# Kernel tuning notes

Measured on AMD Instinct MI355X. Metric: run time of the kernel, lower is better.

## Reference

```python
import jax, jax.numpy as jnp
import numpy as np
import math

B, N, C = 4, 4096, 1024
H, K_LM = 16, 256
HEAD_DIM = C // H


def setup_inputs() -> dict:
    key = jax.random.key(0)
    k1, k2, k3, k4, k5 = jax.random.split(key, 5)
    x = jax.random.normal(k1, (B, N, C), dtype=jnp.float32)
    Wqkv = jax.random.normal(k2, (3 * C, C), dtype=jnp.float32) * 0.02
    E = jax.random.normal(k3, (H, K_LM, N), dtype=jnp.float32) * 0.02
    Wproj = jax.random.normal(k4, (C, C), dtype=jnp.float32) * 0.02
    bproj = jax.random.normal(k5, (C,), dtype=jnp.float32) * 0.02
    return {"x": x, "Wqkv": Wqkv, "E": E, "Wproj": Wproj, "bproj": bproj}


def reference(x, Wqkv, E, Wproj, bproj):
    Bsz, n, c = x.shape
    h, d = H, c // H
    # qkv projection (no bias): [B,N,3C] -> (3,B,H,N,d)
    qkv = (x @ Wqkv.T).reshape(Bsz, n, 3, h, d).transpose(2, 0, 3, 1, 4)
    q, k, v = qkv[0], qkv[1], qkv[2]
    # Linformer landmark projection: E[h,k,n] @ K/V[b,h,n,d] -> [b,h,k,d]
    k_lm = jnp.einsum('hkn,bhnd->bhkd', E, k)
    v_lm = jnp.einsum('hkn,bhnd->bhkd', E, v)
    # scaled dot + softmax over landmarks: [b,h,n,k]
    dot = jnp.einsum('bhnd,bhkd->bhnk', q, k_lm) / math.sqrt(d)
    attn = jax.nn.softmax(dot, axis=-1)
    # weighted sum; faithful to original: reshape (B,H,N,d) -> (B,N,C) WITHOUT head transpose
    out = jnp.einsum('bhnk,bhkd->bhnd', attn, v_lm).reshape(Bsz, n, c)
    # output projection (dropouts are identity at eval / p=0)
    return out @ Wproj.T + bproj
```

## Files before the change

### kernel.cpp

```cpp
#include <hip/hip_runtime.h>


typedef unsigned short ushort_t;
typedef float f32x4 __attribute__((ext_vector_type(4)));
typedef __bf16 bf16x8 __attribute__((ext_vector_type(8)));
typedef unsigned short ushort8 __attribute__((ext_vector_type(8)));
typedef unsigned short ushort4_t __attribute__((ext_vector_type(4)));

__device__ inline ushort_t f2bf(float f) {
  unsigned int u = __float_as_uint(f);
  u += 0x7fff + ((u >> 16) & 1);
  return (ushort_t)(u >> 16);
}

__device__ inline void gload_lds16(const ushort_t* g, ushort_t* l) {
  __builtin_amdgcn_global_load_lds(
      (const __attribute__((address_space(1))) void*)g,
      (__attribute__((address_space(3))) void*)l, 16, 0, 0);
}

__global__ __launch_bounds__(256) void cvt_all(
    const float* __restrict__ x,  ushort_t* __restrict__ xo,
    const float* __restrict__ w1, ushort_t* __restrict__ w1o,
    const float* __restrict__ e,  ushort_t* __restrict__ eo,
    const float* __restrict__ w2, ushort_t* __restrict__ w2o) {
  int i = blockIdx.x * blockDim.x + threadIdx.x;
  const float* in; ushort_t* out; int idx;
  if (i < 4194304)               { in = x;  out = xo;  idx = i; }
  else if (i < 4980736)          { in = w1; out = w1o; idx = i - 4194304; }
  else if (i < 9175040)          { in = e;  out = eo;  idx = i - 4980736; }
  else                           { in = w2; out = w2o; idx = i - 9175040; }
  float4 v = ((const float4*)in)[idx];
  ushort4_t o;
  o.x = f2bf(v.x); o.y = f2bf(v.y); o.z = f2bf(v.z); o.w = f2bf(v.w);
  ((ushort4_t*)out)[idx] = o;
}


#define BARX __builtin_amdgcn_s_barrier()
#define WVM(n) do { asm volatile("s_waitcnt vmcnt(" #n ")" ::: "memory"); \
                    __builtin_amdgcn_sched_barrier(0); } while (0)
#define WLG  do { asm volatile("s_waitcnt lgkmcnt(0)" ::: "memory"); \
                  __builtin_amdgcn_sched_barrier(0); } while (0)

#define STG_A(h, slot, tt) do { \
    gload_lds16(sA[h][0] + (tt) * 64, (ushort_t*)(smem + (slot) * 32768 + (h) * 16384 + (w * 2 + 0) * 1024)); \
    gload_lds16(sA[h][1] + (tt) * 64, (ushort_t*)(smem + (slot) * 32768 + (h) * 16384 + (w * 2 + 1) * 1024)); \
  } while (0)
#define STG_B(h, slot, tt) do { \
    gload_lds16(sB[h][0] + (tt) * 64, (ushort_t*)(smem + 65536 + (slot) * 32768 + (h) * 16384 + (w * 2 + 0) * 1024)); \
    gload_lds16(sB[h][1] + (tt) * 64, (ushort_t*)(smem + 65536 + (slot) * 32768 + (h) * 16384 + (w * 2 + 1) * 1024)); \
  } while (0)

#define RD_A(mh, AF) do { \
    const char* ba_ = smem + sl * 32768 + ((mh) * 128 + wm * 64 + l15) * 128; \
    _Pragma("unroll") for (int i_ = 0; i_ < 4; i_++) { \
      AF[i_][0] = *(const bf16x8*)(ba_ + i_ * 2048 + cs0); \
      AF[i_][1] = *(const bf16x8*)(ba_ + i_ * 2048 + cs1); } \
  } while (0)
#define RD_B(nh) do { \
    const char* bb_ = smem + 65536 + sl * 32768 + ((nh) * 128 + wn * 32 + l15) * 128; \
    _Pragma("unroll") for (int j_ = 0; j_ < 2; j_++) { \
      bF[j_][0] = *(const bf16x8*)(bb_ + j_ * 2048 + cs0); \
      bF[j_][1] = *(const bf16x8*)(bb_ + j_ * 2048 + cs1); } \
  } while (0)

#define MQ(mh, nh, AF) do { \
    _Pragma("unroll") for (int i_ = 0; i_ < 4; i_++) \
    _Pragma("unroll") for (int j_ = 0; j_ < 2; j_++) { \
      acc[(mh) * 4 + i_][(nh) * 2 + j_] = __builtin_amdgcn_mfma_f32_16x16x32_bf16( \
          AF[i_][0], bF[j_][0], acc[(mh) * 4 + i_][(nh) * 2 + j_], 0, 0, 0); \
      acc[(mh) * 4 + i_][(nh) * 2 + j_] = __builtin_amdgcn_mfma_f32_16x16x32_bf16( \
          AF[i_][1], bF[j_][1], acc[(mh) * 4 + i_][(nh) * 2 + j_], 0, 0, 0); } \
  } while (0)

__device__ __attribute__((always_inline)) inline void pipe256(
    const ushort_t* __restrict__ Ag, const ushort_t* __restrict__ Bg,
    long long m0, long long n0, char* smem, f32x4 acc[8][4]) {
  const int tid = threadIdx.x, lane = tid & 63, w = tid >> 6;
  const int l15 = lane & 15, quad = lane >> 4;
  const int wm = w >> 2, wn = w & 3;
  const int sw = l15 & 7;
  const int K = 1024;
  const int cs0 = ((0 * 4 + quad) ^ sw) << 4;
  const int cs1 = ((1 * 4 + quad) ^ sw) << 4;
  const int lr8 = lane >> 3;
  const int sdat = ((lane & 7) ^ lr8) * 8;
  const ushort_t* sA[2][2];
  const ushort_t* sB[2][2];
#pragma unroll
  for (int h = 0; h < 2; h++)
#pragma unroll
    for (int q = 0; q < 2; q++) {
      sA[h][q] = Ag + (m0 + h * 128 + (w * 2 + q) * 8 + lr8) * K + sdat;
      sB[h][q] = Bg + (n0 + h * 128 + (w * 2 + q) * 8 + lr8) * K + sdat;
    }

  const f32x4 zz = {0.f, 0.f, 0.f, 0.f};
#pragma unroll
  for (int i = 0; i < 8; i++)
#pragma unroll
    for (int j = 0; j < 4; j++) acc[i][j] = zz;

  bf16x8 aF0[4][2];
  bf16x8 aF1[4][2];
  bf16x8 bF[2][2];

  STG_A(0, 0, 0); STG_B(0, 0, 0); STG_A(1, 0, 0); STG_B(1, 0, 0);
  WVM(4);
  BARX;

#pragma unroll 2
  for (int t = 0; t < 16; ++t) {
    const int sl = t & 1, sn = sl ^ 1;
    const bool pf = (t < 15);
    RD_A(0, aF0); RD_B(0);
    if (pf) STG_A(0, sn, t + 1);
    BARX; WLG;
    __builtin_amdgcn_s_setprio(1); MQ(0, 0, aF0); __builtin_amdgcn_s_setprio(0);
    if (pf) { WVM(4); } else { WVM(2); }
    BARX;
    RD_A(1, aF1);
    if (pf) STG_B(0, sn, t + 1);
    BARX; WLG;
    __builtin_amdgcn_s_setprio(1); MQ(1, 0, aF1); __builtin_amdgcn_s_setprio(0);
    if (pf) { WVM(4); } else { WVM(0); }
    BARX;
    RD_B(1);
    if (pf) STG_A(1, sn, t + 1);
    BARX; WLG;
    __builtin_amdgcn_s_setprio(1); MQ(1, 1, aF1); __builtin_amdgcn_s_setprio(0);
    BARX;
    if (pf) STG_B(1, sn, t + 1);
    BARX; WLG;
    __builtin_amdgcn_s_setprio(1); MQ(0, 1, aF0); __builtin_amdgcn_s_setprio(0);
    if (pf) WVM(4);
    BARX;
  }
}

__global__ __launch_bounds__(512) void gemm_qkv(
    const ushort_t* __restrict__ A, const ushort_t* __restrict__ W,
    ushort_t* __restrict__ q, ushort_t* __restrict__ kT, ushort_t* __restrict__ vT) {
  __shared__ __align__(16) char smem[131072];
  const int lin = blockIdx.x;
  const int xcd = lin & 7, rr_ = lin >> 3;
  const int mt = xcd * 8 + (rr_ & 7);
  const int nt = rr_ >> 3;
  const long long m0 = (long long)mt * 256;
  const long long n0 = (long long)nt * 256;

  f32x4 acc[8][4];
  pipe256(A, W, m0, n0, smem, acc);

  const int tid = threadIdx.x, lane = tid & 63, w = tid >> 6;
  const int l15 = lane & 15, quad = lane >> 4;
  const int wm = w >> 2, wn = w & 3;
  const int b     = (int)(m0 >> 12);
  const int nrow0 = (int)(m0 & 4095);
  const int s     = (int)(n0 >> 10);
  const int ncol0 = (int)(n0 & 1023);
  const int h0    = ncol0 >> 6;

  if (s == 0) {
#pragma unroll
    for (int mh = 0; mh < 2; mh++)
#pragma unroll
      for (int i = 0; i < 4; i++)
#pragma unroll
        for (int nh = 0; nh < 2; nh++)
#pragma unroll
          for (int j = 0; j < 2; j++) {
            int cx = ncol0 + nh * 128 + wn * 32 + j * 16;
            int h  = cx >> 6;
            int dd = (cx & 63) + l15;
            long long z = (long long)b * 16 + h;
            int nb = nrow0 + mh * 128 + wm * 64 + i * 16 + quad * 4;
#pragma unroll
            for (int r = 0; r < 4; r++)
              q[z * 262144 + (long long)(nb + r) * 64 + dd] = f2bf(acc[mh * 4 + i][nh * 2 + j][r]);
          }
  } else {
    ushort_t (*T)[136] = (ushort_t(*)[136])smem;
    ushort_t* KV = (s == 1) ? kT : vT;
#pragma unroll
    for (int p = 0; p < 2; p++) {
      __syncthreads();
#pragma unroll
      for (int i = 0; i < 4; i++)
#pragma unroll
        for (int nh = 0; nh < 2; nh++)
#pragma unroll
          for (int j = 0; j < 2; j++) {
            int c = nh * 128 + wn * 32 + j * 16 + l15;
            int t = wm * 64 + i * 16 + quad * 4;
            ushort4_t o = {f2bf(acc[p * 4 + i][nh * 2 + j][0]), f2bf(acc[p * 4 + i][nh * 2 + j][1]),
                           f2bf(acc[p * 4 + i][nh * 2 + j][2]), f2bf(acc[p * 4 + i][nh * 2 + j][3])};
            *(ushort4_t*)(&T[c][t]) = o;
          }
      __syncthreads();
#pragma unroll
      for (int it = 0; it < 8; it++) {
        int ch = it * 512 + tid;
        int cl = ch >> 4, tc = (ch & 15) * 8;
        ushort8 v = *(const ushort8*)(&T[cl][tc]);
        int h = h0 + (cl >> 6), dd = cl & 63;
        long long z = (long long)b * 16 + h;
        *(ushort8*)(KV + z * 262144 + (long long)dd * 4096 + (nrow0 + p * 128 + tc)) = v;
      }
    }
  }
}

#define LMSTG(b_, t_) do { \
    ushort_t* base_ = smem + (b_) * 6144; \
    gload_lds16(gE + (t_) * 32, base_ + 512 * w); \
    gload_lds16(gK + (t_) * 32, base_ + 2048 + 512 * w); \
    gload_lds16(gV + (t_) * 32, base_ + 4096 + 512 * w); \
  } while (0)

#define LMCMP(b_) do { \
    const ushort_t* base_ = smem + (b_) * 6144; \
    bf16x8 ef = *(const bf16x8*)(base_ + (w * 16 + l15) * 32 + ((quad ^ swz) * 8)); \
    _Pragma("unroll") for (int j_ = 0; j_ < 4; j_++) { \
      bf16x8 kf = *(const bf16x8*)(base_ + 2048 + (j_ * 16 + l15) * 32 + ((quad ^ swz) * 8)); \
      aK[j_] = __builtin_amdgcn_mfma_f32_16x16x32_bf16(ef, kf, aK[j_], 0, 0, 0); \
      bf16x8 vf = *(const bf16x8*)(base_ + 4096 + (j_ * 16 + l15) * 32 + ((quad ^ swz) * 8)); \
      aV[j_] = __builtin_amdgcn_mfma_f32_16x16x32_bf16(ef, vf, aV[j_], 0, 0, 0); \
    } } while (0)

__global__ __launch_bounds__(256) void lm_gemm(
    const ushort_t* __restrict__ E, const ushort_t* __restrict__ kT,
    const ushort_t* __restrict__ vT, float* __restrict__ pK, float* __restrict__ pV) {
  __shared__ __align__(16) ushort_t smem[12288];
  const int tid = threadIdx.x, lane = tid & 63, w = tid >> 6;
  const int l15 = lane & 15, quad = lane >> 4;
  const int lin = blockIdx.x;
  const int xcd = lin & 7, idx = lin >> 3;
  const int h   = xcd + 8 * (idx >> 6);
  const int rem = idx & 63;
  const int kt  = rem & 3;
  const int zi  = (rem >> 2) & 3;
  const int s   = rem >> 4;
  const int z   = zi * 16 + h;
  const int lr = lane >> 2;
  const int lc = ((lane & 3) ^ ((lr >> 1) & 3)) * 8;
  const int swz = (l15 >> 1) & 3;

  const ushort_t* gE = E  + ((long long)h * 256 + kt * 64 + 16 * w + lr) * 4096 + s * 1024 + lc;
  const ushort_t* gK = kT + ((long long)z * 64 + 16 * w + lr) * 4096 + s * 1024 + lc;
  const ushort_t* gV = vT + ((long long)z * 64 + 16 * w + lr) * 4096 + s * 1024 + lc;

  const f32x4 zz = {0.f, 0.f, 0.f, 0.f};
  f32x4 aK[4], aV[4];
#pragma unroll
  for (int j = 0; j < 4; j++) { aK[j] = zz; aV[j] = zz; }

  LMSTG(0, 0);
#pragma unroll 2
  for (int t = 0; t < 31; ++t) {
    const int b = t & 1;
    LMSTG(b ^ 1, t + 1);
    WVM(3);
    BARX;
    LMCMP(b);
    BARX;
  }
  WVM(0);
  BARX;
  LMCMP(1);

  float* oK = pK + ((long long)(z * 4 + s) * 256 + kt * 64) * 64;
  float* oV = pV + ((long long)(z * 4 + s) * 256 + kt * 64) * 64;
#pragma unroll
  for (int j = 0; j < 4; j++)
#pragma unroll
    for (int r = 0; r < 4; r++) {
      int row = w * 16 + quad * 4 + r, col = j * 16 + l15;
      oK[row * 64 + col] = aK[j][r];
      oV[row * 64 + col] = aV[j][r];
    }
}

__global__ __launch_bounds__(256) void lm_reduce(
    const float* __restrict__ pK, const float* __restrict__ pV,
    ushort_t* __restrict__ klm, ushort_t* __restrict__ vlmT) {
  __shared__ float Tv[64][68];
  const int tid = threadIdx.x;
  const int kt = blockIdx.x;
  const int z  = blockIdx.y;
  const long long base = (long long)z * 4 * 16384 + kt * 64 * 64;
  const int row = tid >> 2, c0 = (tid & 3) * 16;

  float sk[16];
#pragma unroll
  for (int g = 0; g < 4; g++) {
    f32x4 a = {0.f, 0.f, 0.f, 0.f};
#pragma unroll
    for (int s = 0; s < 4; s++)
      a += *(const f32x4*)(pK + base + (long long)s * 16384 + row * 64 + c0 + g * 4);
    sk[g * 4 + 0] = a[0]; sk[g * 4 + 1] = a[1]; sk[g * 4 + 2] = a[2]; sk[g * 4 + 3] = a[3];
  }
  {
    ushort_t* dst = klm + ((long long)z * 256 + kt * 64 + row) * 64 + c0;
    ushort8 o0, o1;
#pragma unroll
    for (int i = 0; i < 8; i++) { o0[i] = f2bf(sk[i]); o1[i] = f2bf(sk[8 + i]); }
    *(ushort8*)(dst) = o0;
    *(ushort8*)(dst + 8) = o1;
  }

#pragma unroll
  for (int g = 0; g < 4; g++) {
    f32x4 a = {0.f, 0.f, 0.f, 0.f};
#pragma unroll
    for (int s = 0; s < 4; s++)
      a += *(const f32x4*)(pV + base + (long long)s * 16384 + row * 64 + c0 + g * 4);
    *(f32x4*)(&Tv[row][c0 + g * 4]) = a;
  }
  __syncthreads();
  {
    ushort8 o0, o1;
#pragma unroll
    for (int i = 0; i < 8; i++) {
      o0[i] = f2bf(Tv[c0 + i][row]);
      o1[i] = f2bf(Tv[c0 + 8 + i][row]);
    }
    ushort_t* dst = vlmT + ((long long)z * 64 + row) * 256 + kt * 64 + c0;
    *(ushort8*)(dst) = o0;
    *(ushort8*)(dst + 8) = o1;
  }
}

__global__ __launch_bounds__(256) void attn_fused(
    const ushort_t* __restrict__ Q, const ushort_t* __restrict__ Klm,
    const ushort_t* __restrict__ VlmT, ushort_t* __restrict__ O) {
  __shared__ __align__(16) ushort_t smem[16896];
  ushort_t (*As)[40]  = (ushort_t(*)[40])smem;
  ushort_t (*Bs)[40]  = (ushort_t(*)[40])(smem + 2560);
  ushort_t (*P)[264]  = (ushort_t(*)[264])smem;
  const int tid = threadIdx.x, lane = tid & 63, w = tid >> 6;
  const int l15 = lane & 15, quad = lane >> 4;
  const int z = blockIdx.z;
  const long long m0 = (long long)blockIdx.x * 64;
  const ushort_t* Qb = Q + (long long)z * 262144;
  const ushort_t* Kb = Klm + (long long)z * 16384;
  const ushort_t* Vb = VlmT + (long long)z * 16384;

  const f32x4 zz = {0.f, 0.f, 0.f, 0.f};
  f32x4 acc[16];
#pragma unroll
  for (int j = 0; j < 16; j++) acc[j] = zz;

  const int sr = tid >> 2, sc = (tid & 3) * 8;

  for (int kt = 0; kt < 2; kt++) {
    const int k0 = kt * 32;
    ushort8 av = *(const ushort8*)(Qb + (m0 + sr) * 64 + k0 + sc);
    ushort8 bv[4];
#pragma unroll
    for (int r = 0; r < 4; r++) {
      int c = r * 256 + tid;
      bv[r] = *(const ushort8*)(Kb + (c >> 2) * 64 + k0 + (c & 3) * 8);
    }
    __syncthreads();
    *(ushort8*)(&As[sr][sc]) = av;
#pragma unroll
    for (int r = 0; r < 4; r++) {
      int c = r * 256 + tid;
      *(ushort8*)(&Bs[c >> 2][(c & 3) * 8]) = bv[r];
    }
    __syncthreads();
    bf16x8 af = *(const bf16x8*)(&As[w * 16 + l15][quad * 8]);
#pragma unroll
    for (int j = 0; j < 16; j++) {
      bf16x8 bfj = *(const bf16x8*)(&Bs[j * 16 + l15][quad * 8]);
      acc[j] = __builtin_amdgcn_mfma_f32_16x16x32_bf16(af, bfj, acc[j], 0, 0, 0);
    }
  }

  __syncthreads();
#pragma unroll
  for (int r = 0; r < 4; r++) {
    float x[16];
    float vmax = -1e30f;
#pragma unroll
    for (int j = 0; j < 16; j++) { x[j] = acc[j][r] * 0.125f; vmax = fmaxf(vmax, x[j]); }
#pragma unroll
    for (int m = 1; m < 16; m <<= 1) vmax = fmaxf(vmax, __shfl_xor(vmax, m, 64));
    float s = 0.f;
#pragma unroll
    for (int j = 0; j < 16; j++) { x[j] = __expf(x[j] - vmax); s += x[j]; }
#pragma unroll
    for (int m = 1; m < 16; m <<= 1) s += __shfl_xor(s, m, 64);
    float inv = 1.0f / s;
    int row = w * 16 + quad * 4 + r;
#pragma unroll
    for (int j = 0; j < 16; j++)
      P[row][j * 16 + l15] = f2bf(x[j] * inv);
  }
  __syncthreads();

  f32x4 o_acc[4];
#pragma unroll
  for (int j = 0; j < 4; j++) o_acc[j] = zz;
#pragma unroll
  for (int kc = 0; kc < 8; kc++) {
    bf16x8 pf = *(const bf16x8*)(&P[w * 16 + l15][kc * 32 + quad * 8]);
#pragma unroll
    for (int j = 0; j < 4; j++) {
      bf16x8 vf = *(const bf16x8*)(Vb + (j * 16 + l15) * 256 + kc * 32 + quad * 8);
      o_acc[j] = __builtin_amdgcn_mfma_f32_16x16x32_bf16(pf, vf, o_acc[j], 0, 0, 0);
    }
  }

#pragma unroll
  for (int j = 0; j < 4; j++)
#pragma unroll
    for (int r = 0; r < 4; r++) {
      int row = w * 16 + quad * 4 + r;
      int col = j * 16 + l15;
      O[(long long)z * 262144 + (m0 + row) * 64 + col] = f2bf(o_acc[j][r]);
    }
}

__global__ __launch_bounds__(512) void gemm_nt_256(
    const ushort_t* __restrict__ A, const ushort_t* __restrict__ B,
    float* __restrict__ C, const float* __restrict__ bias) {
  __shared__ __align__(16) char smem[131072];
  const int lin = blockIdx.x;
  const int xcd = lin & 7, rr_ = lin >> 3;
  const int mt = xcd * 8 + (rr_ & 7);
  const int nt = rr_ >> 3;
  const long long m0 = (long long)mt * 256;
  const long long n0 = (long long)nt * 256;

  f32x4 acc[8][4];
  pipe256(A, B, m0, n0, smem, acc);

  const int tid = threadIdx.x, lane = tid & 63, w = tid >> 6;
  const int l15 = lane & 15, quad = lane >> 4;
  const int wm = w >> 2, wn = w & 3;

#pragma unroll
  for (int mh = 0; mh < 2; mh++)
#pragma unroll
    for (int i = 0; i < 4; i++)
#pragma unroll
      for (int nh = 0; nh < 2; nh++)
#pragma unroll
        for (int j = 0; j < 2; j++) {
          long long row = m0 + mh * 128 + wm * 64 + i * 16 + quad * 4;
          long long col = n0 + nh * 128 + wn * 32 + j * 16 + l15;
          float bv = bias[col];
#pragma unroll
          for (int r = 0; r < 4; r++)
            C[(row + r) * 1024 + col] = acc[mh * 4 + i][nh * 2 + j][r] + bv;
        }
}

extern "C" void kernel_launch(void* const* d_in, const int* in_sizes, int n_in,
                              void* d_out, int out_size, void* d_ws, size_t ws_size,
                              hipStream_t stream) {
  const float* x     = (const float*)d_in[0];
  const float* Wqkv  = (const float*)d_in[1];
  const float* E     = (const float*)d_in[2];
  const float* Wproj = (const float*)d_in[3];
  const float* bproj = (const float*)d_in[4];
  float* out = (float*)d_out;

  char* ws = (char*)d_ws;
  ushort_t* x_bf     = (ushort_t*)(ws + 0);
  float*    pK       = (float*)   (ws + 0);
  float*    pV       = (float*)   (ws + 16777216);
  ushort_t* wqkv_bf  = (ushort_t*)(ws + 33554432);
  ushort_t* e_bf     = (ushort_t*)(ws + 39845888);
  ushort_t* wproj_bf = (ushort_t*)(ws + 73400320);
  ushort_t* q_bf     = (ushort_t*)(ws + 75497472);
  ushort_t* kT       = (ushort_t*)(ws + 109051904);
  ushort_t* vT       = (ushort_t*)(ws + 142606336);
  ushort_t* klm      = (ushort_t*)(ws + 176160768);
  ushort_t* vlmT     = (ushort_t*)(ws + 178257920);

  cvt_all<<<36864, 256, 0, stream>>>(x, x_bf, Wqkv, wqkv_bf, E, e_bf, Wproj, wproj_bf);

  gemm_qkv<<<768, 512, 0, stream>>>(x_bf, wqkv_bf, q_bf, kT, vT);

  lm_gemm<<<1024, 256, 0, stream>>>(e_bf, kT, vT, pK, pV);

  lm_reduce<<<dim3(4, 64), 256, 0, stream>>>(pK, pV, klm, vlmT);

  attn_fused<<<dim3(64, 1, 64), 256, 0, stream>>>(q_bf, klm, vlmT, x_bf);

  gemm_nt_256<<<256, 512, 0, stream>>>(x_bf, wproj_bf, out, bproj);
}
```

Before: 420.9 us.

## Enlarge lm_gemm tile to all 256 landmarks with 3-stage LDS pipeline

Each lm_gemm block now covers all 256 landmark rows with 8 waves, not a 64-row slice, so the K/V tiles are loaded once per block rather than four times across separate blocks. Each wave computes two 16-row E fragments against shared K/V fragments. The prefetch ring goes from double to triple buffering with a deeper wait count. The cost is 4x fewer blocks (256), which is about one block per CU, so there is less latency hiding across blocks, plus higher LDS use (72KB) and more accumulator registers.

```diff
diff --git a/kernel.cpp b/kernel.cpp
--- a/kernel.cpp
+++ b/kernel.cpp
@@ -213,73 +213,79 @@
 }
 
 #define LMSTG(b_, t_) do { \
-    ushort_t* base_ = smem + (b_) * 6144; \
-    gload_lds16(gE + (t_) * 32, base_ + 512 * w); \
-    gload_lds16(gK + (t_) * 32, base_ + 2048 + 512 * w); \
-    gload_lds16(gV + (t_) * 32, base_ + 4096 + 512 * w); \
+    ushort_t* bb = smem + (b_) * 12288; \
+    gload_lds16(gE0 + (t_) * 32, bb + w * 1024); \
+    gload_lds16(gE1 + (t_) * 32, bb + w * 1024 + 512); \
+    gload_lds16(gKV + (t_) * 32, bb + 8192 + w * 512); \
   } while (0)
 
 #define LMCMP(b_) do { \
-    const ushort_t* base_ = smem + (b_) * 6144; \
-    bf16x8 ef = *(const bf16x8*)(base_ + (w * 16 + l15) * 32 + ((quad ^ swz) * 8)); \
+    const ushort_t* bb = smem + (b_) * 12288; \
+    bf16x8 ef0 = *(const bf16x8*)(bb + (w * 32 + l15) * 32 + ((quad ^ swz) * 8)); \
+    bf16x8 ef1 = *(const bf16x8*)(bb + (w * 32 + 16 + l15) * 32 + ((quad ^ swz) * 8)); \
     _Pragma("unroll") for (int j_ = 0; j_ < 4; j_++) { \
-      bf16x8 kf = *(const bf16x8*)(base_ + 2048 + (j_ * 16 + l15) * 32 + ((quad ^ swz) * 8)); \
-      aK[j_] = __builtin_amdgcn_mfma_f32_16x16x32_bf16(ef, kf, aK[j_], 0, 0, 0); \
-      bf16x8 vf = *(const bf16x8*)(base_ + 4096 + (j_ * 16 + l15) * 32 + ((quad ^ swz) * 8)); \
-      aV[j_] = __builtin_amdgcn_mfma_f32_16x16x32_bf16(ef, vf, aV[j_], 0, 0, 0); \
+      bf16x8 kf = *(const bf16x8*)(bb + 8192 + (j_ * 16 + l15) * 32 + ((quad ^ swz) * 8)); \
+      aK[0][j_] = __builtin_amdgcn_mfma_f32_16x16x32_bf16(ef0, kf, aK[0][j_], 0, 0, 0); \
+      aK[1][j_] = __builtin_amdgcn_mfma_f32_16x16x32_bf16(ef1, kf, aK[1][j_], 0, 0, 0); \
+      bf16x8 vf = *(const bf16x8*)(bb + 10240 + (j_ * 16 + l15) * 32 + ((quad ^ swz) * 8)); \
+      aV[0][j_] = __builtin_amdgcn_mfma_f32_16x16x32_bf16(ef0, vf, aV[0][j_], 0, 0, 0); \
+      aV[1][j_] = __builtin_amdgcn_mfma_f32_16x16x32_bf16(ef1, vf, aV[1][j_], 0, 0, 0); \
     } } while (0)
 
-__global__ __launch_bounds__(256) void lm_gemm(
+__global__ __launch_bounds__(512) void lm_gemm(
     const ushort_t* __restrict__ E, const ushort_t* __restrict__ kT,
     const ushort_t* __restrict__ vT, float* __restrict__ pK, float* __restrict__ pV) {
-  __shared__ __align__(16) ushort_t smem[12288];
+  __shared__ __align__(16) ushort_t smem[36864];
   const int tid = threadIdx.x, lane = tid & 63, w = tid >> 6;
   const int l15 = lane & 15, quad = lane >> 4;
   const int lin = blockIdx.x;
   const int xcd = lin & 7, idx = lin >> 3;
-  const int h   = xcd + 8 * (idx >> 6);
-  const int rem = idx & 63;
-  const int kt  = rem & 3;
-  const int zi  = (rem >> 2) & 3;
-  const int s   = rem >> 4;
+  const int h   = xcd + 8 * (idx >> 4);
+  const int rem = idx & 15;
+  const int zi  = rem & 3;
+  const int s   = rem >> 2;
   const int z   = zi * 16 + h;
   const int lr = lane >> 2;
   const int lc = ((lane & 3) ^ ((lr >> 1) & 3)) * 8;
   const int swz = (l15 >> 1) & 3;
 
-  const ushort_t* gE = E  + ((long long)h * 256 + kt * 64 + 16 * w + lr) * 4096 + s * 1024 + lc;
-  const ushort_t* gK = kT + ((long long)z * 64 + 16 * w + lr) * 4096 + s * 1024 + lc;
-  const ushort_t* gV = vT + ((long long)z * 64 + 16 * w + lr) * 4096 + s * 1024 + lc;
+  const ushort_t* gE0 = E + ((long long)h * 256 + w * 32 + lr) * 4096 + s * 1024 + lc;
+  const ushort_t* gE1 = gE0 + 16 * 4096;
+  const ushort_t* gKV = (w < 4)
+      ? kT + ((long long)z * 64 + w * 16 + lr) * 4096 + s * 1024 + lc
+      : vT + ((long long)z * 64 + (w - 4) * 16 + lr) * 4096 + s * 1024 + lc;
 
   const f32x4 zz = {0.f, 0.f, 0.f, 0.f};
-  f32x4 aK[4], aV[4];
-#pragma unroll
-  for (int j = 0; j < 4; j++) { aK[j] = zz; aV[j] = zz; }
-
-  LMSTG(0, 0);
-#pragma unroll 2
-  for (int t = 0; t < 31; ++t) {
-    const int b = t & 1;
-    LMSTG(b ^ 1, t + 1);
-    WVM(3);
+  f32x4 aK[2][4], aV[2][4];
+#pragma unroll
+  for (int f = 0; f < 2; f++)
+#pragma unroll
+    for (int j = 0; j < 4; j++) { aK[f][j] = zz; aV[f][j] = zz; }
+
+  LMSTG(0, 0); LMSTG(1, 1);
+#pragma unroll 3
+  for (int t = 0; t < 30; ++t) {
+    LMSTG((t + 2) % 3, t + 2);
+    WVM(6);
     BARX;
-    LMCMP(b);
+    LMCMP(t % 3);
     BARX;
   }
-  WVM(0);
-  BARX;
-  LMCMP(1);
-
-  float* oK = pK + ((long long)(z * 4 + s) * 256 + kt * 64) * 64;
-  float* oV = pV + ((long long)(z * 4 + s) * 256 + kt * 64) * 64;
-#pragma unroll
-  for (int j = 0; j < 4; j++)
-#pragma unroll
-    for (int r = 0; r < 4; r++) {
-      int row = w * 16 + quad * 4 + r, col = j * 16 + l15;
-      oK[row * 64 + col] = aK[j][r];
-      oV[row * 64 + col] = aV[j][r];
-    }
+  WVM(3); BARX; LMCMP(0);  BARX;
+  WVM(0); BARX; LMCMP(1);
+
+  float* oK = pK + (long long)(z * 4 + s) * 16384;
+  float* oV = pV + (long long)(z * 4 + s) * 16384;
+#pragma unroll
+  for (int f = 0; f < 2; f++)
+#pragma unroll
+    for (int j = 0; j < 4; j++)
+#pragma unroll
+      for (int r = 0; r < 4; r++) {
+        int row = w * 32 + f * 16 + quad * 4 + r, col = j * 16 + l15;
+        oK[row * 64 + col] = aK[f][j][r];
+        oV[row * 64 + col] = aV[f][j][r];
+      }
 }
 
 __global__ __launch_bounds__(256) void lm_reduce(
@@ -486,7 +492,7 @@
 
   gemm_qkv<<<768, 512, 0, stream>>>(x_bf, wqkv_bf, q_bf, kT, vT);
 
-  lm_gemm<<<1024, 256, 0, stream>>>(e_bf, kT, vT, pK, pV);
+  lm_gemm<<<256, 512, 0, stream>>>(e_bf, kT, vT, pK, pV);
 
   lm_reduce<<<dim3(4, 64), 256, 0, stream>>>(pK, pV, klm, vlmT);
 
```

New measurement: 434.5 us. +3.2%, slower.
